# Performance work log

Hardware: AMD Instinct MI355X
Metric: run time of the kernel (lower is better)

The kernel has to match this reference:

```python
import jax, jax.numpy as jnp
import numpy as np

B, S, D_IN = 4, 2048, 1024
N_HEAD, D_ATTN, D_OUT = 16, 64, 1024
D_H = N_HEAD * D_ATTN  # 1024; NOTE: no head split in original module


def setup_inputs() -> dict:
    key = jax.random.key(0)
    ks = jax.random.split(key, 12)
    s = 1.0 / np.sqrt(D_IN)
    inp = {
        "q": jax.random.normal(ks[0], (B, S, D_IN), dtype=jnp.float32),
        "k": jax.random.normal(ks[1], (B, S, D_IN), dtype=jnp.float32),
        "v": jax.random.normal(ks[2], (B, S, D_IN), dtype=jnp.float32),
        "mask": jax.random.randint(ks[3], (B, S, S), 0, 2, dtype=jnp.int32),
        "Wq": jax.random.normal(ks[4], (D_H, D_IN), dtype=jnp.float32) * s,
        "bq": jnp.zeros((D_H,), dtype=jnp.float32),
        "Wk": jax.random.normal(ks[5], (D_H, D_IN), dtype=jnp.float32) * s,
        "bk": jnp.zeros((D_H,), dtype=jnp.float32),
        "Wv": jax.random.normal(ks[6], (D_H, D_IN), dtype=jnp.float32) * s,
        "bv": jnp.zeros((D_H,), dtype=jnp.float32),
        "Wo": jax.random.normal(ks[7], (D_OUT, D_H), dtype=jnp.float32) * (1.0 / np.sqrt(D_H)),
        "bo": jnp.zeros((D_OUT,), dtype=jnp.float32),
    }
    return inp


def reference(q, k, v, mask, Wq, bq, Wk, bk, Wv, bv, Wo, bo):
    # manual QKV projections (torch Linear: x @ W.T + b)
    Q = q @ Wq.T + bq  # [B,S,D_H]
    K = k @ Wk.T + bk
    V = v @ Wv.T + bv
    d_k = Q.shape[-1]  # full concatenated dim (no head split, faithful)
    e = jnp.einsum("bsd,btd->bst", Q, K) / jnp.sqrt(jnp.float32(d_k))  # [B,S,S]
    MASK_FILL = jnp.float32(-(2 ** 15))  # original uses -2**15 regardless of dtype
    e = jnp.where(mask == 0, MASK_FILL, e)
    a = jax.nn.softmax(e, axis=-1)
    y = jnp.einsum("bst,btd->bsd", a, V)  # [B,S,D_H]
    return y @ Wo.T + bo  # [B,S,D_OUT]
```

## Files before the change

### kernel.cpp

```cpp
#include <hip/hip_runtime.h>
#include <hip/hip_bf16.h>

#define B_   4
#define S_   2048
#define DIN  1024
#define DH   1024
#define DOUT 1024

typedef __attribute__((ext_vector_type(8))) __bf16 bf16x8;
typedef __attribute__((ext_vector_type(4))) float floatx4;
typedef unsigned short u16;
typedef unsigned int u32;
typedef unsigned long long u64;

__device__ inline u16 f2bf(float f) {
  union { float f; u32 u; } x; x.f = f;
  u32 r = x.u + 0x7fffu + ((x.u >> 16) & 1u);
  return (u16)(r >> 16);
}

#define GLOAD(SRC, DST) __builtin_amdgcn_global_load_lds(                     \
    (const __attribute__((address_space(1))) u32*)(SRC),                      \
    (__attribute__((address_space(3))) u32*)(DST), 16, 0, 0)
#define WAITVM0() asm volatile("s_waitcnt vmcnt(0)" ::: "memory")

__global__ __launch_bounds__(256)
void prep(const float* __restrict__ q, const float* __restrict__ k,
          const float* __restrict__ v, const float* __restrict__ w0,
          const float* __restrict__ w1, const float* __restrict__ w2,
          const float* __restrict__ w3, u16* __restrict__ dst,
          const int* __restrict__ mask, u64* __restrict__ packed,
          const float* __restrict__ b0, const float* __restrict__ b1,
          const float* __restrict__ b2, float* __restrict__ bcat) {
  const long nQ = (long)B_ * S_ * DIN;
  const long nW = (long)DH * DIN;
  long b = blockIdx.x;
  if (b < 28672) {
    const float* src; long doff;
    if (b < 8192)       { src = q;  doff = 0;            }
    else if (b < 16384) { src = k;  doff = nQ;     b -= 8192;  }
    else if (b < 24576) { src = v;  doff = 2 * nQ; b -= 16384; }
    else if (b < 25600) { src = w0; doff = 3 * nQ; b -= 24576; }
    else if (b < 26624) { src = w1; doff = 3 * nQ + nW;     b -= 25600; }
    else if (b < 27648) { src = w2; doff = 3 * nQ + 2 * nW; b -= 26624; }
    else                { src = w3; doff = 3 * nQ + 3 * nW; b -= 27648; }
    long i = b * 256 + threadIdx.x;
    float4 vv = ((const float4*)src)[i];
    ushort4 o;
    o.x = f2bf(vv.x); o.y = f2bf(vv.y); o.z = f2bf(vv.z); o.w = f2bf(vv.w);
    ((ushort4*)(dst + doff))[i] = o;
  } else if (b < 94208) {
    const long i = (b - 28672) * 256 + threadIdx.x;
    const int mk = mask[i];
    const u64 bal = __ballot(mk != 0);
    if ((threadIdx.x & 63) == 0) packed[i >> 6] = bal;
  } else {
    int i = (int)(b - 94208) * 256 + threadIdx.x;
    if (i < DH) bcat[i] = b0[i];
    else if (i < 2 * DH) bcat[i] = b1[i - DH];
    else if (i < 3 * DH) bcat[i] = b2[i - 2 * DH];
  }
}

__global__ __launch_bounds__(256)
void transpose_bf16(const u16* __restrict__ in, u16* __restrict__ out) {
  __shared__ u16 t[32][33];
  const int b = blockIdx.z;
  const int r0 = blockIdx.y * 32, c0 = blockIdx.x * 32;
  const int tx = threadIdx.x & 31, ty = threadIdx.x >> 5;
  const u16* ib = in + (long)b * S_ * DH;
  u16* ob = out + (long)b * DH * S_;
#pragma unroll
  for (int i = 0; i < 4; ++i) {
    int r = ty + i * 8;
    t[r][tx] = ib[(long)(r0 + r) * DH + (c0 + tx)];
  }
  __syncthreads();
#pragma unroll
  for (int i = 0; i < 4; ++i) {
    int r = ty + i * 8;
    ob[(long)(c0 + r) * S_ + (r0 + tx)] = t[tx][r];
  }
}

#define EPI_BF16_BIAS     0
#define EPI_BF16_ROWSCALE 1
#define EPI_F32_BIAS      2

template <int EPI>
__global__ __launch_bounds__(256, 4)
void gemm97(const u16* __restrict__ A, const u16* __restrict__ Bm,
            void* __restrict__ C, const float* __restrict__ bias,
            const float* __restrict__ Psum,
            int M, int N, int K,
            long sA, long sB, long sC, long sBias,
            int nbx, int nby) {
  __shared__ u16 lds_[16384];
  __shared__ float invs_s[(EPI == EPI_BF16_ROWSCALE) ? 128 : 1];

  const int tid = threadIdx.x;
  const int w = tid >> 6, l = tid & 63;
  const int wr = w >> 1, wc = w & 1;
  const int lr = l & 15, q = l >> 4;

  const int flat = blockIdx.x;
  const int swz = (flat & 7) * ((int)gridDim.x >> 3) + (flat >> 3);
  const int bx = swz % nbx;
  const int rest = swz / nbx;
  const int by = rest % nby;
  const int bz = rest / nby;

  const long arow0 = (long)by * 128;
  const long bcol0 = (long)bx * 128;
  const u16* Ab = A + bz * sA + arow0 * K;
  const u16* Bb = Bm + bz * sB + bcol0 * K;
  const int nt = K >> 6;

  if constexpr (EPI == EPI_BF16_ROWSCALE) {
    if (tid < 128) {
      const float4* p = (const float4*)(Psum + ((long)bz * S_ + arow0 + tid) * 16);
      float4 a = p[0], b = p[1], c = p[2], d = p[3];
      float s = (a.x + a.y + a.z + a.w) + (b.x + b.y + b.z + b.w)
              + (c.x + c.y + c.z + c.w) + (d.x + d.y + d.z + d.w);
      invs_s[tid] = 1.0f / s;
    }
  }

  const int st_r = tid >> 3;
  const int st_ks = (tid & 7) ^ (st_r & 7);

  floatx4 acc[4][4] = {};

  for (int t = 0; t < nt; ++t) {
    const long k0 = (long)t << 6;
#pragma unroll
    for (int i = 0; i < 4; ++i)
      GLOAD(Ab + (long)(i * 32 + st_r) * K + k0 + st_ks * 8,
            &lds_[i * 2048 + tid * 8]);
#pragma unroll
    for (int i = 0; i < 4; ++i)
      GLOAD(Bb + (long)(i * 32 + st_r) * K + k0 + st_ks * 8,
            &lds_[8192 + i * 2048 + tid * 8]);
    WAITVM0();
    __syncthreads();

    bf16x8 a[4][2], b[4][2];
#pragma unroll
    for (int m = 0; m < 4; ++m)
#pragma unroll
      for (int kk = 0; kk < 2; ++kk) {
        const int r = wr * 64 + m * 16 + lr, s = kk * 4 + q;
        a[m][kk] = *(const bf16x8*)&lds_[r * 64 + ((s ^ (r & 7)) * 8)];
      }
#pragma unroll
    for (int n = 0; n < 4; ++n)
#pragma unroll
      for (int kk = 0; kk < 2; ++kk) {
        const int c = wc * 64 + n * 16 + lr, s = kk * 4 + q;
        b[n][kk] = *(const bf16x8*)&lds_[8192 + c * 64 + ((s ^ (c & 7)) * 8)];
      }
#pragma unroll
    for (int kk = 0; kk < 2; ++kk)
#pragma unroll
      for (int n = 0; n < 4; ++n)
#pragma unroll
        for (int m = 0; m < 4; ++m)
          acc[m][n] = __builtin_amdgcn_mfma_f32_16x16x32_bf16(
              a[m][kk], b[n][kk], acc[m][n], 0, 0, 0);
    __syncthreads();
  }

  const int r4 = q * 4;
#pragma unroll
  for (int mf = 0; mf < 4; ++mf)
#pragma unroll
    for (int nf = 0; nf < 4; ++nf)
#pragma unroll
      for (int r = 0; r < 4; ++r) {
        const long row = arow0 + wr * 64 + mf * 16 + r4 + r;
        const long col = bcol0 + wc * 64 + nf * 16 + lr;
        float v = acc[mf][nf][r];
        if constexpr (EPI == EPI_BF16_BIAS) {
          v += bias[bz * sBias + col];
          ((u16*)C)[bz * sC + row * N + col] = f2bf(v);
        } else if constexpr (EPI == EPI_BF16_ROWSCALE) {
          v *= invs_s[wr * 64 + mf * 16 + r4 + r];
          ((u16*)C)[bz * sC + row * N + col] = f2bf(v);
        } else {
          v += bias[col];
          ((float*)C)[bz * sC + row * N + col] = v;
        }
      }
}

__global__ __launch_bounds__(256, 4)
void pexp128(const u16* __restrict__ Q, const u16* __restrict__ Kb_,
             u16* __restrict__ P, const u32* __restrict__ packed,
             float* __restrict__ Psum) {
  __shared__ u16 lds_[16384];

  const int tid = threadIdx.x;
  const int w = tid >> 6, l = tid & 63;
  const int wr = w >> 1, wc = w & 1;
  const int lr = l & 15, q = l >> 4;

  const int flat = blockIdx.x;
  const int swz = (flat & 7) * ((int)gridDim.x >> 3) + (flat >> 3);
  const int bx = swz & 15;
  const int rest = swz >> 4;
  const int by = rest & 15;
  const int bz = rest >> 4;

  const long arow0 = (long)by * 128;
  const long bcol0 = (long)bx * 128;
  const int K = DH;
  const u16* Ab = Q + (long)bz * S_ * DH + arow0 * K;
  const u16* Bb = Kb_ + (long)bz * S_ * DH + bcol0 * K;

  const int st_r = tid >> 3;
  const int st_ks = (tid & 7) ^ (st_r & 7);

  floatx4 acc[4][4] = {};

#pragma unroll 4
  for (int t = 0; t < 16; ++t) {
    const long k0 = (long)t << 6;
#pragma unroll
    for (int i = 0; i < 4; ++i)
      GLOAD(Ab + (long)(i * 32 + st_r) * K + k0 + st_ks * 8,
            &lds_[i * 2048 + tid * 8]);
#pragma unroll
    for (int i = 0; i < 4; ++i)
      GLOAD(Bb + (long)(i * 32 + st_r) * K + k0 + st_ks * 8,
            &lds_[8192 + i * 2048 + tid * 8]);
    WAITVM0();
    __syncthreads();

    bf16x8 a[4][2], b[4][2];
#pragma unroll
    for (int m = 0; m < 4; ++m)
#pragma unroll
      for (int kk = 0; kk < 2; ++kk) {
        const int r = wr * 64 + m * 16 + lr, s = kk * 4 + q;
        a[m][kk] = *(const bf16x8*)&lds_[r * 64 + ((s ^ (r & 7)) * 8)];
      }
#pragma unroll
    for (int n = 0; n < 4; ++n)
#pragma unroll
      for (int kk = 0; kk < 2; ++kk) {
        const int c = wc * 64 + n * 16 + lr, s = kk * 4 + q;
        b[n][kk] = *(const bf16x8*)&lds_[8192 + c * 64 + ((s ^ (c & 7)) * 8)];
      }
#pragma unroll
    for (int kk = 0; kk < 2; ++kk)
#pragma unroll
      for (int n = 0; n < 4; ++n)
#pragma unroll
        for (int m = 0; m < 4; ++m)
          acc[m][n] = __builtin_amdgcn_mfma_f32_16x16x32_bf16(
              a[m][kk], b[n][kk], acc[m][n], 0, 0, 0);
    __syncthreads();
  }

  u32* pw = (u32*)&lds_[8192];
  {
    const u32* pg = packed + (long)bz * S_ * (S_ / 32)
                  + arow0 * (S_ / 32) + (bcol0 >> 5);
    const int lrow = tid >> 1;
    const int j0 = (tid & 1) * 2;
    pw[lrow * 4 + j0]     = pg[(long)lrow * (S_ / 32) + j0];
    pw[lrow * 4 + j0 + 1] = pg[(long)lrow * (S_ / 32) + j0 + 1];
  }
  __syncthreads();

  const int r4 = q * 4;
  float rsum[4][4];
#pragma unroll
  for (int mf = 0; mf < 4; ++mf)
#pragma unroll
    for (int r = 0; r < 4; ++r) rsum[mf][r] = 0.f;

#pragma unroll
  for (int mf = 0; mf < 4; ++mf)
#pragma unroll
    for (int r = 0; r < 4; ++r) {
      const int lrow = wr * 64 + mf * 16 + r4 + r;
      const long row = arow0 + lrow;
#pragma unroll
      for (int nf = 0; nf < 4; ++nf) {
        const u32 word = pw[lrow * 4 + wc * 2 + (nf >> 1)];
        const int bitpos = (nf & 1) * 16 + lr;
        const long col = bcol0 + wc * 64 + nf * 16 + lr;
        float p = 0.f;
        if ((word >> bitpos) & 1u) p = __expf(acc[mf][nf][r] * 0.03125f);
        P[(long)bz * S_ * S_ + row * S_ + col] = f2bf(p);
        rsum[mf][r] += p;
      }
    }
  __syncthreads();

  float* sc = (float*)lds_;
#pragma unroll
  for (int mf = 0; mf < 4; ++mf)
#pragma unroll
    for (int r = 0; r < 4; ++r) {
      float s = rsum[mf][r];
      s += __shfl_xor(s, 1); s += __shfl_xor(s, 2);
      s += __shfl_xor(s, 4); s += __shfl_xor(s, 8);
      if (lr == 0) sc[(wr * 64 + mf * 16 + r4 + r) * 2 + wc] = s;
    }
  __syncthreads();
  if (tid < 128) {
    float tot = sc[tid * 2] + sc[tid * 2 + 1];
    Psum[((long)bz * S_ + arow0 + tid) * 16 + bx] = tot;
  }
}

extern "C" void kernel_launch(void* const* d_in, const int* in_sizes, int n_in,
                              void* d_out, int out_size, void* d_ws, size_t ws_size,
                              hipStream_t stream) {
  const float* q    = (const float*)d_in[0];
  const float* k    = (const float*)d_in[1];
  const float* v    = (const float*)d_in[2];
  const int*   mask = (const int*)d_in[3];
  const float* Wq   = (const float*)d_in[4];
  const float* bq   = (const float*)d_in[5];
  const float* Wk   = (const float*)d_in[6];
  const float* bk   = (const float*)d_in[7];
  const float* Wv   = (const float*)d_in[8];
  const float* bv   = (const float*)d_in[9];
  const float* Wo   = (const float*)d_in[10];
  const float* bo   = (const float*)d_in[11];

  const long BS = (long)B_ * S_;
  const long nQ = BS * DH;
  const long nW = (long)DH * DIN;
  const long nE = (long)B_ * S_ * S_;

  char* ws = (char*)d_ws;
  size_t off = 0;
  auto alloc = [&](size_t bytes) {
    void* p = ws + off; off += (bytes + 255) & ~(size_t)255; return p;
  };

  u16* qb   = (u16*)alloc(nQ * 2);
  u16* kb   = (u16*)alloc(nQ * 2);
  u16* vb   = (u16*)alloc(nQ * 2);
  u16* wqb  = (u16*)alloc(nW * 2);
  u16* wkb  = (u16*)alloc(nW * 2);
  u16* wvb  = (u16*)alloc(nW * 2);
  u16* wob  = (u16*)alloc(nW * 2);
  u16* Qb   = (u16*)alloc(nQ * 2);
  u16* Kbf  = (u16*)alloc(nQ * 2);
  u16* Vb   = (u16*)alloc(nQ * 2);
  u16* VT   = (u16*)alloc(nQ * 2);
  u16* P    = (u16*)alloc(nE * 2);
  u64* pk   = (u64*)alloc(nE / 8);
  float* Psum = (float*)alloc(BS * 16 * 4);
  float* bcat = (float*)alloc(3 * DH * 4);
  u16* Yb  = vb;
  (void)kb; (void)wkb; (void)wvb;

  prep<<<dim3(94220), 256, 0, stream>>>(q, k, v, Wq, Wk, Wv, Wo, qb,
                                        mask, pk, bq, bk, bv, bcat);

  gemm97<EPI_BF16_BIAS><<<dim3(1536), 256, 0, stream>>>(qb, wqb, Qb, bcat,
      nullptr, (int)BS, DH, DIN, nQ, nW, nQ, DH, 8, 64);

  {
    dim3 g(DH / 32, S_ / 32, B_);
    transpose_bf16<<<g, 256, 0, stream>>>(Vb, VT);
  }

  pexp128<<<dim3(1024), 256, 0, stream>>>(Qb, Kbf, P, (const u32*)pk, Psum);

  gemm97<EPI_BF16_ROWSCALE><<<dim3(512), 256, 0, stream>>>(P, VT, Yb,
      nullptr, Psum, S_, DH, S_,
      (long)S_ * S_, (long)DH * S_, (long)S_ * DH, 0, 8, 16);

  gemm97<EPI_F32_BIAS><<<dim3(512), 256, 0, stream>>>(Yb, wob, d_out, bo,
      nullptr, (int)BS, DOUT, DH, 0, 0, 0, 0, 8, 64);
}
```

Baseline: 233.2 us.

## Use grid-stride prep with vectorized int4 mask packing and new bit layout

The prep kernel changes from one block per 256 elements (about 94k blocks) to a fixed grid of 1804 blocks that loop with a grid stride. The mask is now read as int4 per thread and packed with four ballots into an interleaved bitmask layout. The attention-exp kernel's mask lookup is rewritten to match the new bit ordering. This cuts block launch overhead and widens the mask loads, but the permuted bitmask layout must be decoded exactly right in the consumer.

```diff
diff --git a/kernel.cpp b/kernel.cpp
--- a/kernel.cpp
+++ b/kernel.cpp
@@ -34,28 +34,47 @@
           const float* __restrict__ b2, float* __restrict__ bcat) {
   const long nQ = (long)B_ * S_ * DIN;
   const long nW = (long)DH * DIN;
-  long b = blockIdx.x;
-  if (b < 28672) {
-    const float* src; long doff;
-    if (b < 8192)       { src = q;  doff = 0;            }
-    else if (b < 16384) { src = k;  doff = nQ;     b -= 8192;  }
-    else if (b < 24576) { src = v;  doff = 2 * nQ; b -= 16384; }
-    else if (b < 25600) { src = w0; doff = 3 * nQ; b -= 24576; }
-    else if (b < 26624) { src = w1; doff = 3 * nQ + nW;     b -= 25600; }
-    else if (b < 27648) { src = w2; doff = 3 * nQ + 2 * nW; b -= 26624; }
-    else                { src = w3; doff = 3 * nQ + 3 * nW; b -= 27648; }
-    long i = b * 256 + threadIdx.x;
-    float4 vv = ((const float4*)src)[i];
-    ushort4 o;
-    o.x = f2bf(vv.x); o.y = f2bf(vv.y); o.z = f2bf(vv.z); o.w = f2bf(vv.w);
-    ((ushort4*)(dst + doff))[i] = o;
-  } else if (b < 94208) {
-    const long i = (b - 28672) * 256 + threadIdx.x;
-    const int mk = mask[i];
-    const u64 bal = __ballot(mk != 0);
-    if ((threadIdx.x & 63) == 0) packed[i >> 6] = bal;
+  const long nQ4 = nQ >> 2;
+  const long nW4 = nW >> 2;
+  const int b = blockIdx.x;
+
+  if (b < 1536) {
+    const long total4 = 3 * nQ4 + 4 * nW4;
+    for (long i = (long)b * 256 + threadIdx.x; i < total4; i += 1536L * 256) {
+      const float* src; long doff, idx;
+      if (i < nQ4)               { src = q;  doff = 0;          idx = i; }
+      else if (i < 2 * nQ4)      { src = k;  doff = nQ;         idx = i - nQ4; }
+      else if (i < 3 * nQ4)      { src = v;  doff = 2 * nQ;     idx = i - 2 * nQ4; }
+      else {
+        long j = i - 3 * nQ4;
+        if (j < nW4)             { src = w0; doff = 3 * nQ;          idx = j; }
+        else if (j < 2 * nW4)    { src = w1; doff = 3 * nQ + nW;     idx = j - nW4; }
+        else if (j < 3 * nW4)    { src = w2; doff = 3 * nQ + 2 * nW; idx = j - 2 * nW4; }
+        else                     { src = w3; doff = 3 * nQ + 3 * nW; idx = j - 3 * nW4; }
+      }
+      float4 vv = ((const float4*)src)[idx];
+      ushort4 o;
+      o.x = f2bf(vv.x); o.y = f2bf(vv.y); o.z = f2bf(vv.z); o.w = f2bf(vv.w);
+      ((ushort4*)(dst + doff))[idx] = o;
+    }
+  } else if (b < 1792) {
+    const long nI4 = ((long)B_ * S_ * S_) >> 2;
+    for (long f = (long)(b - 1536) * 256 + threadIdx.x; f < nI4; f += 256L * 256) {
+      int4 m4 = ((const int4*)mask)[f];
+      u64 bal0 = __ballot(m4.x != 0);
+      u64 bal1 = __ballot(m4.y != 0);
+      u64 bal2 = __ballot(m4.z != 0);
+      u64 bal3 = __ballot(m4.w != 0);
+      if ((threadIdx.x & 63) == 0) {
+        const long g = f >> 6;
+        ulonglong2 p01; p01.x = bal0; p01.y = bal1;
+        ulonglong2 p23; p23.x = bal2; p23.y = bal3;
+        ((ulonglong2*)(packed + g * 4))[0] = p01;
+        ((ulonglong2*)(packed + g * 4))[1] = p23;
+      }
+    }
   } else {
-    int i = (int)(b - 94208) * 256 + threadIdx.x;
+    int i = (b - 1792) * 256 + threadIdx.x;
     if (i < DH) bcat[i] = b0[i];
     else if (i < 2 * DH) bcat[i] = b1[i - DH];
     else if (i < 3 * DH) bcat[i] = b2[i - 2 * DH];
@@ -264,12 +283,12 @@
 
   u32* pw = (u32*)&lds_[8192];
   {
-    const u32* pg = packed + (long)bz * S_ * (S_ / 32)
-                  + arow0 * (S_ / 32) + (bcol0 >> 5);
+    const int half = bx & 1;
     const int lrow = tid >> 1;
     const int j0 = (tid & 1) * 2;
-    pw[lrow * 4 + j0]     = pg[(long)lrow * (S_ / 32) + j0];
-    pw[lrow * 4 + j0 + 1] = pg[(long)lrow * (S_ / 32) + j0 + 1];
+    const long g = (long)bz * 16384 + (arow0 + lrow) * 8 + (bx >> 1);
+    pw[lrow * 4 + j0]     = packed[g * 8 + j0 * 2 + half];
+    pw[lrow * 4 + j0 + 1] = packed[g * 8 + (j0 + 1) * 2 + half];
   }
   __syncthreads();
 
@@ -286,10 +305,10 @@
     for (int r = 0; r < 4; ++r) {
       const int lrow = wr * 64 + mf * 16 + r4 + r;
       const long row = arow0 + lrow;
+      const u32 word = pw[lrow * 4 + (lr & 3)];
 #pragma unroll
       for (int nf = 0; nf < 4; ++nf) {
-        const u32 word = pw[lrow * 4 + wc * 2 + (nf >> 1)];
-        const int bitpos = (nf & 1) * 16 + lr;
+        const int bitpos = wc * 16 + nf * 4 + (lr >> 2);
         const long col = bcol0 + wc * 64 + nf * 16 + lr;
         float p = 0.f;
         if ((word >> bitpos) & 1u) p = __expf(acc[mf][nf][r] * 0.03125f);
@@ -361,8 +380,8 @@
   u16* Yb  = vb;
   (void)kb; (void)wkb; (void)wvb;
 
-  prep<<<dim3(94220), 256, 0, stream>>>(q, k, v, Wq, Wk, Wv, Wo, qb,
-                                        mask, pk, bq, bk, bv, bcat);
+  prep<<<dim3(1804), 256, 0, stream>>>(q, k, v, Wq, Wk, Wv, Wo, qb,
+                                       mask, pk, bq, bk, bv, bcat);
 
   gemm97<EPI_BF16_BIAS><<<dim3(1536), 256, 0, stream>>>(qb, wqb, Qb, bcat,
       nullptr, (int)BS, DH, DIN, nQ, nW, nQ, DH, 8, 64);
```

Result: no change. 229.3 us (-1.7%).
